# Kernel optimization log

Hardware: AMD Instinct MI355X
Metric: run time of the kernel (lower is better)

The kernel has to match this reference:

```python
import jax, jax.numpy as jnp
import numpy as np

B = 128          # persons in the batch
V = 300          # visits per person (< MAX_VISITS so all kept)
MAX_VISITS = 510 # 512 - 2, hard-coded in the module
D = 256          # embedding_dim * n_heads
VOCAB = 50000
MAX_DAYS = 365


def setup_inputs() -> dict:
    key = jax.random.key(0)
    k_codes, k_times, k_emb = jax.random.split(key, 3)

    total_visits = B * V  # 38400
    v = np.arange(total_visits)
    codes_per_visit = 8 + (v % 8)                      # 8..15 codes per visit
    code_to_visit = np.repeat(v, codes_per_visit).astype(np.int32)  # sorted segment ids (sum_indices)
    total_codes = code_to_visit.shape[0]               # 441600
    visit_person = (v // V).astype(np.int32)
    visit_slot = (MAX_VISITS - V + (v % V)).astype(np.int32)  # right-aligned slots

    all_codes = jax.random.randint(k_codes, (total_codes,), 0, VOCAB, dtype=jnp.int32)
    times = jax.random.uniform(k_times, (total_visits,), dtype=jnp.float32) * (MAX_DAYS - 1)
    concept_emb = jax.random.normal(k_emb, (VOCAB, D), dtype=jnp.float32)
    pad_embedding = jnp.zeros((D,), dtype=jnp.float32)  # torch.nn.Parameter(torch.zeros(D))
    # ((1/10000) ** (1/D)) ** range(D//2)
    timescales = jnp.asarray(((1.0 / 10000.0) ** (1.0 / D)) ** np.arange(D // 2), dtype=jnp.float32)

    return {
        "all_codes": all_codes,
        "code_to_visit": jnp.asarray(code_to_visit),
        "visit_person": jnp.asarray(visit_person),
        "visit_slot": jnp.asarray(visit_slot),
        "times": times,
        "concept_emb": concept_emb,
        "pad_embedding": pad_embedding,
        "timescales": timescales,
    }


def reference(all_codes, code_to_visit, visit_person, visit_slot, times,
              concept_emb, pad_embedding, timescales):
    total_visits = visit_person.shape[0]
    d = concept_emb.shape[1]

    # concept-embedding gather: [total_codes, D]
    embedded_raw = concept_emb[all_codes]

    # per-visit segment sum (index_add_): [total_visits, D]
    summed = jax.ops.segment_sum(embedded_raw, code_to_visit,
                                 num_segments=total_visits,
                                 indices_are_sorted=True)

    # padded tensor initialised with pad_embedding, then right-aligned scatter of visits
    base = jnp.zeros((B, MAX_VISITS, d), dtype=summed.dtype) + pad_embedding
    reshaped = base.at[visit_person, visit_slot].set(summed)

    # sinusoidal time embedding: cat(sin(t*ts), cos(t*ts))
    t = jnp.clip(times, 0.0, MAX_DAYS - 1)
    ang = t[:, None] * timescales[None, :]                       # [total_visits, D/2]
    temb_un = jnp.concatenate([jnp.sin(ang), jnp.cos(ang)], 1)   # [total_visits, D]
    time_embedding = jnp.zeros((B, MAX_VISITS, d), dtype=summed.dtype)
    time_embedding = time_embedding.at[visit_person, visit_slot].set(temb_un)

    return reshaped + time_embedding
```

## Files before the change

kernel.cpp:

```cpp
#include <hip/hip_runtime.h>

#define MAXV 510
#define D4 64

typedef float floatx4 __attribute__((ext_vector_type(4)));

__device__ __forceinline__ unsigned int pack2_bf16_rne(float a, float b) {
    unsigned int ua = __builtin_bit_cast(unsigned int, a);
    unsigned int ub = __builtin_bit_cast(unsigned int, b);
    ua = (ua + 0x7FFFu + ((ua >> 16) & 1u)) >> 16;
    ub = (ub + 0x7FFFu + ((ub >> 16) & 1u)) >> 16;
    return ua | (ub << 16);
}

__device__ __forceinline__ float bf_lo(unsigned int u) {
    return __builtin_bit_cast(float, u << 16);
}
__device__ __forceinline__ float bf_hi(unsigned int u) {
    return __builtin_bit_cast(float, u & 0xFFFF0000u);
}

__device__ __forceinline__ void acc8(floatx4& a0, floatx4& a1, uint4 u) {
    a0.x += bf_lo(u.x); a0.y += bf_hi(u.x);
    a0.z += bf_lo(u.y); a0.w += bf_hi(u.y);
    a1.x += bf_lo(u.z); a1.y += bf_hi(u.z);
    a1.z += bf_lo(u.w); a1.w += bf_hi(u.w);
}

__device__ __forceinline__ float fast_sin(float x) {
    float r = x * 0.15915494309189535f;
    r = r - floorf(r);
    return __builtin_amdgcn_sinf(r);
}
__device__ __forceinline__ float fast_cos(float x) {
    float r = x * 0.15915494309189535f;
    r = r - floorf(r);
    return __builtin_amdgcn_cosf(r);
}

__device__ __forceinline__ int lower_bound_i(const int* __restrict__ a,
                                             int lo, int hi, int key) {
    while (lo < hi) {
        int m = (lo + hi) >> 1;
        if (a[m] < key) lo = m + 1; else hi = m;
    }
    return lo;
}

__global__ __launch_bounds__(256) void prep(
    const floatx4* __restrict__ in, uint4* __restrict__ outtab, int npairs,
    const int* __restrict__ c2v,
    const int* __restrict__ person,
    const int* __restrict__ slot,
    const float* __restrict__ times,
    int4* __restrict__ rec,
    int total_codes, int total_visits)
{
    const int i = blockIdx.x * blockDim.x + threadIdx.x;

    if (i < total_visits) {
        const int lo = lower_bound_i(c2v, 0, total_codes, i);
        const int hi = lower_bound_i(c2v, lo, total_codes, i + 1);
        int4 r;
        r.x = lo;
        r.y = hi - lo;
        r.z = __builtin_bit_cast(int, times[i]);
        r.w = 0;
        rec[person[i] * MAXV + slot[i]] = r;
    }

    if (i < npairs) {
        const floatx4 a = __builtin_nontemporal_load(&in[2 * i]);
        const floatx4 b = __builtin_nontemporal_load(&in[2 * i + 1]);
        uint4 r;
        r.x = pack2_bf16_rne(a.x, a.y);
        r.y = pack2_bf16_rne(a.z, a.w);
        r.z = pack2_bf16_rne(b.x, b.y);
        r.w = pack2_bf16_rne(b.z, b.w);
        outtab[i] = r;
    }
}

__global__ __launch_bounds__(256) void fused_bf16(
    const int* __restrict__ all_codes,
    const uint4* __restrict__ embh,
    const floatx4* __restrict__ pad,
    const floatx4* __restrict__ tsc,
    const int4* __restrict__ rec,
    floatx4* __restrict__ out,
    int nslots)
{
    const int tid = threadIdx.x;
    const int w = tid >> 6;
    const int lane = tid & 63;
    const int half = lane >> 5;
    const int hl = lane & 31;
    const int slot_id = blockIdx.x * 4 + w;
    if (slot_id >= nslots) return;

    const int4 rc = rec[slot_id];
    if (rc.x < 0) {
        __builtin_nontemporal_store(pad[lane], &out[slot_id * D4 + lane]);
        return;
    }
    const int lo = rc.x;
    const int cnt = rc.y;
    const int rmax = cnt - 1;

    int mycode = 0;
    if (cnt > 0) mycode = all_codes[lo + min(lane, rmax)];

    const int f = 2 * hl + half;
    float t = __builtin_bit_cast(float, rc.z);
    t = fminf(fmaxf(t, 0.f), 364.f);
    const floatx4 ts = tsc[f & 31];
    floatx4 tv;
    if (f < 32) {
        tv.x = fast_sin(t * ts.x); tv.y = fast_sin(t * ts.y);
        tv.z = fast_sin(t * ts.z); tv.w = fast_sin(t * ts.w);
    } else {
        tv.x = fast_cos(t * ts.x); tv.y = fast_cos(t * ts.y);
        tv.z = fast_cos(t * ts.z); tv.w = fast_cos(t * ts.w);
    }

    floatx4 acc0 = (floatx4)(0.f);
    floatx4 acc1 = (floatx4)(0.f);

    if (cnt > 0) {
        if (cnt <= 16) {
            if (cnt <= 8) {
                const int c0 = __shfl(mycode, min(half,     rmax));
                const int c1 = __shfl(mycode, min(2 + half, rmax));
                const int c2 = __shfl(mycode, min(4 + half, rmax));
                const int c3 = __shfl(mycode, min(6 + half, rmax));
                const uint4 e0 = embh[(size_t)c0 * 32 + hl];
                const uint4 e1 = embh[(size_t)c1 * 32 + hl];
                const uint4 e2 = embh[(size_t)c2 * 32 + hl];
                const uint4 e3 = embh[(size_t)c3 * 32 + hl];
                if (half     < cnt) acc8(acc0, acc1, e0);
                if (2 + half < cnt) acc8(acc0, acc1, e1);
                if (4 + half < cnt) acc8(acc0, acc1, e2);
                if (6 + half < cnt) acc8(acc0, acc1, e3);
            } else {
                const int c0 = __shfl(mycode, half);
                const int c1 = __shfl(mycode, 2 + half);
                const int c2 = __shfl(mycode, 4 + half);
                const int c3 = __shfl(mycode, 6 + half);
                const int c4 = __shfl(mycode, min(8  + half, rmax));
                const int c5 = __shfl(mycode, min(10 + half, rmax));
                const int c6 = __shfl(mycode, min(12 + half, rmax));
                const int c7 = __shfl(mycode, min(14 + half, rmax));
                const uint4 e0 = embh[(size_t)c0 * 32 + hl];
                const uint4 e1 = embh[(size_t)c1 * 32 + hl];
                const uint4 e2 = embh[(size_t)c2 * 32 + hl];
                const uint4 e3 = embh[(size_t)c3 * 32 + hl];
                const uint4 e4 = embh[(size_t)c4 * 32 + hl];
                const uint4 e5 = embh[(size_t)c5 * 32 + hl];
                const uint4 e6 = embh[(size_t)c6 * 32 + hl];
                const uint4 e7 = embh[(size_t)c7 * 32 + hl];
                acc8(acc0, acc1, e0);
                acc8(acc0, acc1, e1);
                acc8(acc0, acc1, e2);
                acc8(acc0, acc1, e3);
                if (8  + half < cnt) acc8(acc0, acc1, e4);
                if (10 + half < cnt) acc8(acc0, acc1, e5);
                if (12 + half < cnt) acc8(acc0, acc1, e6);
                if (14 + half < cnt) acc8(acc0, acc1, e7);
            }
        } else if (cnt <= 64) {
            for (int j = 0; j < cnt; j += 8) {
                const int j0 = j + half;
                const int j1 = j + 2 + half;
                const int j2 = j + 4 + half;
                const int j3 = j + 6 + half;
                const int c0 = __shfl(mycode, min(j0, rmax));
                const int c1 = __shfl(mycode, min(j1, rmax));
                const int c2 = __shfl(mycode, min(j2, rmax));
                const int c3 = __shfl(mycode, min(j3, rmax));
                const uint4 e0 = embh[(size_t)c0 * 32 + hl];
                const uint4 e1 = embh[(size_t)c1 * 32 + hl];
                const uint4 e2 = embh[(size_t)c2 * 32 + hl];
                const uint4 e3 = embh[(size_t)c3 * 32 + hl];
                if (j0 < cnt) acc8(acc0, acc1, e0);
                if (j1 < cnt) acc8(acc0, acc1, e1);
                if (j2 < cnt) acc8(acc0, acc1, e2);
                if (j3 < cnt) acc8(acc0, acc1, e3);
            }
        } else {
            for (int j = 0; j < cnt; j += 2) {
                const int jj = min(j + half, cnt - 1);
                const int c = all_codes[lo + jj];
                const uint4 e = embh[(size_t)c * 32 + hl];
                if (j + half < cnt) acc8(acc0, acc1, e);
            }
        }
    }

    acc0.x += __shfl_xor(acc0.x, 32); acc0.y += __shfl_xor(acc0.y, 32);
    acc0.z += __shfl_xor(acc0.z, 32); acc0.w += __shfl_xor(acc0.w, 32);
    acc1.x += __shfl_xor(acc1.x, 32); acc1.y += __shfl_xor(acc1.y, 32);
    acc1.z += __shfl_xor(acc1.z, 32); acc1.w += __shfl_xor(acc1.w, 32);

    floatx4 r = half ? acc1 : acc0;
    r.x += tv.x; r.y += tv.y; r.z += tv.z; r.w += tv.w;

    __builtin_nontemporal_store(r, &out[slot_id * D4 + f]);
}

__global__ __launch_bounds__(256) void build_maps(
    const int* __restrict__ c2v,
    const int* __restrict__ person,
    const int* __restrict__ slot,
    int* __restrict__ inv,
    int* __restrict__ off,
    int total_codes, int total_visits)
{
    int v = blockIdx.x * blockDim.x + threadIdx.x;
    if (v >= total_visits) return;
    inv[person[v] * MAXV + slot[v]] = v;
    int lo = 0, hi = total_codes;
    while (lo < hi) {
        int m = (lo + hi) >> 1;
        if (c2v[m] < v) lo = m + 1; else hi = m;
    }
    off[v] = lo;
    if (v == 0) off[total_visits] = total_codes;
}

__global__ __launch_bounds__(256) void fused_f32(
    const int* __restrict__ all_codes,
    const float* __restrict__ times,
    const floatx4* __restrict__ emb,
    const floatx4* __restrict__ pad,
    const floatx4* __restrict__ tsc,
    const int* __restrict__ inv,
    const int* __restrict__ off,
    floatx4* __restrict__ out,
    int nslots)
{
    const int tid = threadIdx.x;
    const int w = tid >> 6;
    const int lane = tid & 63;
    const int slot_id = blockIdx.x * 4 + w;
    if (slot_id >= nslots) return;

    const int v = inv[slot_id];
    if (v < 0) {
        __builtin_nontemporal_store(pad[lane], &out[slot_id * D4 + lane]);
        return;
    }
    const int lo = off[v];
    const int hi = off[v + 1];

    float t = times[v];
    t = fminf(fmaxf(t, 0.f), 364.f);
    const floatx4 ts = tsc[lane & 31];
    floatx4 acc;
    if (lane < 32) {
        acc.x = sinf(t * ts.x); acc.y = sinf(t * ts.y);
        acc.z = sinf(t * ts.z); acc.w = sinf(t * ts.w);
    } else {
        acc.x = cosf(t * ts.x); acc.y = cosf(t * ts.y);
        acc.z = cosf(t * ts.z); acc.w = cosf(t * ts.w);
    }
    for (int i = lo; i < hi; ++i)
        acc += emb[(size_t)all_codes[i] * D4 + lane];
    __builtin_nontemporal_store(acc, &out[slot_id * D4 + lane]);
}

extern "C" void kernel_launch(void* const* d_in, const int* in_sizes, int n_in,
                              void* d_out, int out_size, void* d_ws, size_t ws_size,
                              hipStream_t stream) {
    const int*   all_codes = (const int*)d_in[0];
    const int*   c2v       = (const int*)d_in[1];
    const int*   person    = (const int*)d_in[2];
    const int*   slot      = (const int*)d_in[3];
    const float* times     = (const float*)d_in[4];
    const float* emb       = (const float*)d_in[5];
    const float* pad       = (const float*)d_in[6];
    const float* tsc       = (const float*)d_in[7];

    const int total_codes  = in_sizes[0];
    const int total_visits = in_sizes[2];
    const int emb_elems    = in_sizes[5];
    const int nslots       = out_size / 256;

    char* ws = (char*)d_ws;
    int4* rec = (int4*)ws;
    size_t head = ((size_t)nslots * sizeof(int4) + 255) & ~(size_t)255;
    unsigned short* embh = (unsigned short*)(ws + head);
    const size_t needed = head + (size_t)emb_elems * sizeof(unsigned short);

    if (ws_size >= needed) {
        const int npairs = emb_elems / 8;
        const int nthreads = max(npairs, total_visits);
        prep<<<(nthreads + 255) / 256, 256, 0, stream>>>(
            (const floatx4*)emb, (uint4*)embh, npairs,
            c2v, person, slot, times, rec, total_codes, total_visits);
        fused_bf16<<<(nslots + 3) / 4, 256, 0, stream>>>(
            all_codes, (const uint4*)embh, (const floatx4*)pad,
            (const floatx4*)tsc, rec, (floatx4*)d_out, nslots);
    } else {
        int* inv = (int*)ws;
        int* off = inv + nslots;
        (void)hipMemsetAsync(inv, 0xFF, (size_t)nslots * sizeof(int), stream);
        build_maps<<<(total_visits + 255) / 256, 256, 0, stream>>>(
            c2v, person, slot, inv, off, total_codes, total_visits);
        fused_f32<<<(nslots + 3) / 4, 256, 0, stream>>>(
            all_codes, times, (const floatx4*)emb, (const floatx4*)pad,
            (const floatx4*)tsc, inv, off, (floatx4*)d_out, nslots);
    }
}
```

Measured before the change: 158.3 us.

## Pack per-slot visit codes into 64-byte records to remove dependent code loads

```diff
diff --git a/kernel.cpp b/kernel.cpp
--- a/kernel.cpp
+++ b/kernel.cpp
@@ -49,11 +49,12 @@
 
 __global__ __launch_bounds__(256) void prep(
     const floatx4* __restrict__ in, uint4* __restrict__ outtab, int npairs,
+    const int* __restrict__ all_codes,
     const int* __restrict__ c2v,
     const int* __restrict__ person,
     const int* __restrict__ slot,
     const float* __restrict__ times,
-    int4* __restrict__ rec,
+    uint4* __restrict__ rec,
     int total_codes, int total_visits)
 {
     const int i = blockIdx.x * blockDim.x + threadIdx.x;
@@ -61,12 +62,28 @@
     if (i < total_visits) {
         const int lo = lower_bound_i(c2v, 0, total_codes, i);
         const int hi = lower_bound_i(c2v, lo, total_codes, i + 1);
-        int4 r;
-        r.x = lo;
-        r.y = hi - lo;
-        r.z = __builtin_bit_cast(int, times[i]);
-        r.w = 0;
-        rec[person[i] * MAXV + slot[i]] = r;
+        const int cnt = hi - lo;
+
+        unsigned int w[16];
+        w[0] = __builtin_bit_cast(unsigned int, times[i]);
+        if (cnt <= 15) {
+            const unsigned int c0 = (cnt > 0) ? (unsigned int)all_codes[lo] : 0u;
+            w[1] = ((unsigned int)cnt << 26) | (c0 & 0x3FFFFFFu);
+            #pragma unroll
+            for (int k = 1; k < 15; ++k)
+                w[k + 1] = (k < cnt) ? (unsigned int)all_codes[lo + k] : 0u;
+        } else {
+            w[1] = (31u << 26) | ((unsigned int)lo & 0x3FFFFFFu);
+            w[2] = (unsigned int)cnt;
+            #pragma unroll
+            for (int k = 3; k < 16; ++k) w[k] = 0u;
+        }
+
+        uint4* dst = rec + (size_t)(person[i] * MAXV + slot[i]) * 4;
+        dst[0] = make_uint4(w[0],  w[1],  w[2],  w[3]);
+        dst[1] = make_uint4(w[4],  w[5],  w[6],  w[7]);
+        dst[2] = make_uint4(w[8],  w[9],  w[10], w[11]);
+        dst[3] = make_uint4(w[12], w[13], w[14], w[15]);
     }
 
     if (i < npairs) {
@@ -86,7 +103,7 @@
     const uint4* __restrict__ embh,
     const floatx4* __restrict__ pad,
     const floatx4* __restrict__ tsc,
-    const int4* __restrict__ rec,
+    const unsigned int* __restrict__ rec,
     floatx4* __restrict__ out,
     int nslots)
 {
@@ -98,20 +115,61 @@
     const int slot_id = blockIdx.x * 4 + w;
     if (slot_id >= nslots) return;
 
-    const int4 rc = rec[slot_id];
-    if (rc.x < 0) {
+    const unsigned int myw = rec[(size_t)slot_id * 16 + (lane & 15)];
+    const unsigned int cw = ((lane & 15) == 1) ? (myw & 0x3FFFFFFu) : myw;
+
+    const int w1 = __shfl((int)myw, 1);
+    if (w1 < 0) {
         __builtin_nontemporal_store(pad[lane], &out[slot_id * D4 + lane]);
         return;
     }
-    const int lo = rc.x;
-    const int cnt = rc.y;
-    const int rmax = cnt - 1;
-
-    int mycode = 0;
-    if (cnt > 0) mycode = all_codes[lo + min(lane, rmax)];
+
+    const unsigned int tag = ((unsigned int)w1) >> 26;
+    floatx4 acc0 = (floatx4)(0.f);
+    floatx4 acc1 = (floatx4)(0.f);
+
+    if (tag != 31u) {
+        const int cnt = (int)tag;
+        if (cnt > 0) {
+            const int rmax = cnt - 1;
+            const int c0 = (int)__shfl((int)cw, min(half,      rmax) + 1);
+            const int c1 = (int)__shfl((int)cw, min(2 + half,  rmax) + 1);
+            const int c2 = (int)__shfl((int)cw, min(4 + half,  rmax) + 1);
+            const int c3 = (int)__shfl((int)cw, min(6 + half,  rmax) + 1);
+            const int c4 = (int)__shfl((int)cw, min(8 + half,  rmax) + 1);
+            const int c5 = (int)__shfl((int)cw, min(10 + half, rmax) + 1);
+            const int c6 = (int)__shfl((int)cw, min(12 + half, rmax) + 1);
+            const int c7 = (int)__shfl((int)cw, min(14 + half, rmax) + 1);
+            const uint4 e0 = embh[(size_t)c0 * 32 + hl];
+            const uint4 e1 = embh[(size_t)c1 * 32 + hl];
+            const uint4 e2 = embh[(size_t)c2 * 32 + hl];
+            const uint4 e3 = embh[(size_t)c3 * 32 + hl];
+            const uint4 e4 = embh[(size_t)c4 * 32 + hl];
+            const uint4 e5 = embh[(size_t)c5 * 32 + hl];
+            const uint4 e6 = embh[(size_t)c6 * 32 + hl];
+            const uint4 e7 = embh[(size_t)c7 * 32 + hl];
+            if (half      < cnt) acc8(acc0, acc1, e0);
+            if (2 + half  < cnt) acc8(acc0, acc1, e1);
+            if (4 + half  < cnt) acc8(acc0, acc1, e2);
+            if (6 + half  < cnt) acc8(acc0, acc1, e3);
+            if (8 + half  < cnt) acc8(acc0, acc1, e4);
+            if (10 + half < cnt) acc8(acc0, acc1, e5);
+            if (12 + half < cnt) acc8(acc0, acc1, e6);
+            if (14 + half < cnt) acc8(acc0, acc1, e7);
+        }
+    } else {
+        const int lo = w1 & 0x3FFFFFF;
+        const int cnt = (int)__shfl((int)myw, 2);
+        for (int j = 0; j < cnt; j += 2) {
+            const int jj = min(j + half, cnt - 1);
+            const int c = all_codes[lo + jj];
+            const uint4 e = embh[(size_t)c * 32 + hl];
+            if (j + half < cnt) acc8(acc0, acc1, e);
+        }
+    }
 
     const int f = 2 * hl + half;
-    float t = __builtin_bit_cast(float, rc.z);
+    float t = __builtin_bit_cast(float, __shfl((int)myw, 0));
     t = fminf(fmaxf(t, 0.f), 364.f);
     const floatx4 ts = tsc[f & 31];
     floatx4 tv;
@@ -121,79 +179,6 @@
     } else {
         tv.x = fast_cos(t * ts.x); tv.y = fast_cos(t * ts.y);
         tv.z = fast_cos(t * ts.z); tv.w = fast_cos(t * ts.w);
-    }
-
-    floatx4 acc0 = (floatx4)(0.f);
-    floatx4 acc1 = (floatx4)(0.f);
-
-    if (cnt > 0) {
-        if (cnt <= 16) {
-            if (cnt <= 8) {
-                const int c0 = __shfl(mycode, min(half,     rmax));
-                const int c1 = __shfl(mycode, min(2 + half, rmax));
-                const int c2 = __shfl(mycode, min(4 + half, rmax));
-                const int c3 = __shfl(mycode, min(6 + half, rmax));
-                const uint4 e0 = embh[(size_t)c0 * 32 + hl];
-                const uint4 e1 = embh[(size_t)c1 * 32 + hl];
-                const uint4 e2 = embh[(size_t)c2 * 32 + hl];
-                const uint4 e3 = embh[(size_t)c3 * 32 + hl];
-                if (half     < cnt) acc8(acc0, acc1, e0);
-                if (2 + half < cnt) acc8(acc0, acc1, e1);
-                if (4 + half < cnt) acc8(acc0, acc1, e2);
-                if (6 + half < cnt) acc8(acc0, acc1, e3);
-            } else {
-                const int c0 = __shfl(mycode, half);
-                const int c1 = __shfl(mycode, 2 + half);
-                const int c2 = __shfl(mycode, 4 + half);
-                const int c3 = __shfl(mycode, 6 + half);
-                const int c4 = __shfl(mycode, min(8  + half, rmax));
-                const int c5 = __shfl(mycode, min(10 + half, rmax));
-                const int c6 = __shfl(mycode, min(12 + half, rmax));
-                const int c7 = __shfl(mycode, min(14 + half, rmax));
-                const uint4 e0 = embh[(size_t)c0 * 32 + hl];
-                const uint4 e1 = embh[(size_t)c1 * 32 + hl];
-                const uint4 e2 = embh[(size_t)c2 * 32 + hl];
-                const uint4 e3 = embh[(size_t)c3 * 32 + hl];
-                const uint4 e4 = embh[(size_t)c4 * 32 + hl];
-                const uint4 e5 = embh[(size_t)c5 * 32 + hl];
-                const uint4 e6 = embh[(size_t)c6 * 32 + hl];
-                const uint4 e7 = embh[(size_t)c7 * 32 + hl];
-                acc8(acc0, acc1, e0);
-                acc8(acc0, acc1, e1);
-                acc8(acc0, acc1, e2);
-                acc8(acc0, acc1, e3);
-                if (8  + half < cnt) acc8(acc0, acc1, e4);
-                if (10 + half < cnt) acc8(acc0, acc1, e5);
-                if (12 + half < cnt) acc8(acc0, acc1, e6);
-                if (14 + half < cnt) acc8(acc0, acc1, e7);
-            }
-        } else if (cnt <= 64) {
-            for (int j = 0; j < cnt; j += 8) {
-                const int j0 = j + half;
-                const int j1 = j + 2 + half;
-                const int j2 = j + 4 + half;
-                const int j3 = j + 6 + half;
-                const int c0 = __shfl(mycode, min(j0, rmax));
-                const int c1 = __shfl(mycode, min(j1, rmax));
-                const int c2 = __shfl(mycode, min(j2, rmax));
-                const int c3 = __shfl(mycode, min(j3, rmax));
-                const uint4 e0 = embh[(size_t)c0 * 32 + hl];
-                const uint4 e1 = embh[(size_t)c1 * 32 + hl];
-                const uint4 e2 = embh[(size_t)c2 * 32 + hl];
-                const uint4 e3 = embh[(size_t)c3 * 32 + hl];
-                if (j0 < cnt) acc8(acc0, acc1, e0);
-                if (j1 < cnt) acc8(acc0, acc1, e1);
-                if (j2 < cnt) acc8(acc0, acc1, e2);
-                if (j3 < cnt) acc8(acc0, acc1, e3);
-            }
-        } else {
-            for (int j = 0; j < cnt; j += 2) {
-                const int jj = min(j + half, cnt - 1);
-                const int c = all_codes[lo + jj];
-                const uint4 e = embh[(size_t)c * 32 + hl];
-                if (j + half < cnt) acc8(acc0, acc1, e);
-            }
-        }
     }
 
     acc0.x += __shfl_xor(acc0.x, 32); acc0.y += __shfl_xor(acc0.y, 32);
@@ -286,8 +271,8 @@
     const int nslots       = out_size / 256;
 
     char* ws = (char*)d_ws;
-    int4* rec = (int4*)ws;
-    size_t head = ((size_t)nslots * sizeof(int4) + 255) & ~(size_t)255;
+    uint4* rec = (uint4*)ws;
+    size_t head = ((size_t)nslots * 64 + 255) & ~(size_t)255;
     unsigned short* embh = (unsigned short*)(ws + head);
     const size_t needed = head + (size_t)emb_elems * sizeof(unsigned short);
 
@@ -296,10 +281,12 @@
         const int nthreads = max(npairs, total_visits);
         prep<<<(nthreads + 255) / 256, 256, 0, stream>>>(
             (const floatx4*)emb, (uint4*)embh, npairs,
-            c2v, person, slot, times, rec, total_codes, total_visits);
+            all_codes, c2v, person, slot, times, rec,
+            total_codes, total_visits);
         fused_bf16<<<(nslots + 3) / 4, 256, 0, stream>>>(
             all_codes, (const uint4*)embh, (const floatx4*)pad,
-            (const floatx4*)tsc, rec, (floatx4*)d_out, nslots);
+            (const floatx4*)tsc, (const unsigned int*)rec,
+            (floatx4*)d_out, nslots);
     } else {
         int* inv = (int*)ws;
         int* off = inv + nslots;
```

Result: no change. 159.6 us (+0.8%).
